# Performance work log

Measured on AMD Instinct MI355X. Metric: run time of the kernel, lower is better.

The kernel has to match this reference:

```python
import jax, jax.numpy as jnp
import numpy as np


def haar_dwt2d(x):
    """Orthonormal 2D Haar DWT. x: [B,C,H,W] -> (LL, LH, HL, HH) each [B,C,H/2,W/2].
    Matches conv2d(stride=2) with dec_lo=[1/sqrt2,1/sqrt2], dec_hi=[-1/sqrt2,1/sqrt2]."""
    x00 = x[:, :, 0::2, 0::2]
    x01 = x[:, :, 0::2, 1::2]
    x10 = x[:, :, 1::2, 0::2]
    x11 = x[:, :, 1::2, 1::2]
    LL = (x00 + x01 + x10 + x11) * 0.5
    LH = (x10 + x11 - x00 - x01) * 0.5  # high-pass along H
    HL = (x01 + x11 - x00 - x10) * 0.5  # high-pass along W
    HH = (x00 - x01 - x10 + x11) * 0.5
    return LL, LH, HL, HH


def haar_idwt2d(LL, LH, HL, HH):
    """Exact inverse of haar_dwt2d. Each input [B,C,h,w] -> [B,C,2h,2w]."""
    x00 = (LL - LH - HL + HH) * 0.5
    x01 = (LL - LH + HL - HH) * 0.5
    x10 = (LL + LH - HL - HH) * 0.5
    x11 = (LL + LH + HL + HH) * 0.5
    B, C, h, w = LL.shape
    row0 = jnp.stack([x00, x01], axis=-1).reshape(B, C, h, 2 * w)
    row1 = jnp.stack([x10, x11], axis=-1).reshape(B, C, h, 2 * w)
    return jnp.stack([row0, row1], axis=-2).reshape(B, C, 2 * h, 2 * w)


def _gate(t, thr):
    # scalar 0/1 gate: subband kept iff max|t| > thr (no grad through the gate)
    return (jnp.max(jnp.abs(t)) > thr).astype(t.dtype)


def reference(x):
    # WaveletTree: tree_level=8, sr_ratio=2, method='root', use_thres=True, threshold=1
    thr = jnp.asarray(1.0, dtype=x.dtype)

    LL1, LH1, HL1, HH1 = haar_dwt2d(x)
    LL2, LH2, HL2, HH2 = haar_dwt2d(LL1)
    LL3, LH3, HL3, HH3 = haar_dwt2d(LL2)

    # level-3 gates
    g3_lh = _gate(LH3, thr)
    g3_hl = _gate(HL3, thr)
    g3_hh = _gate(HH3, thr)
    out = haar_idwt2d(LL3, LH3 * g3_lh, HL3 * g3_hl, HH3 * g3_hh)

    # level-2 gates ('root' method: child kept only if parent was kept)
    thr2 = thr * 0.5
    g2_lh = _gate(LH2, thr2) * g3_lh
    g2_hl = _gate(HL2, thr2) * g3_hl
    g2_hh = _gate(HH2, thr2) * g3_hh
    out = haar_idwt2d(out, LH2 * g2_lh, HL2 * g2_hl, HH2 * g2_hh)

    # level-1 gated elementwise adds
    thr1 = thr * 0.25
    g1_lh = _gate(LH1, thr1) * g2_lh
    g1_hl = _gate(HL1, thr1) * g2_hl
    g1_hh = _gate(HH1, thr1) * g2_hh
    out = out + LH1 * g1_lh + HL1 * g1_hl + HH1 * g1_hh
    return out  # [B, C, H/2, W/2]


def setup_inputs() -> dict:
    key = jax.random.key(0)
    x = jax.random.normal(key, (8, 192, 224, 224), dtype=jnp.float32)
    return {"x": x}
```

## Files before the change

### kernel.cpp

```cpp
#include <hip/hip_runtime.h>


#define IMG_W 224
#define OUT_W 112
#define BANDS_PER_IMG 28
#define BAND_FLOATS 1792
#define OUT_BAND_FLOATS 448
#define NBG 1536
#define NBR 1024
#define WS_SLOTS 64

__device__ __forceinline__ void fwd_quad(float a, float b, float c, float d,
                                         float& ll, float& lh, float& hl, float& hh) {
    ll = (a + b + c + d) * 0.5f;
    lh = (c + d - a - b) * 0.5f;
    hl = (b + d - a - c) * 0.5f;
    hh = (a - b - c + d) * 0.5f;
}

__global__ __launch_bounds__(256, 6) void wav_gate_kernel(const float* __restrict__ x,
                                                          int* __restrict__ ws,
                                                          int n_bands) {
    const int lane = (int)threadIdx.x & 63;
    const int y = lane >> 4;
    const int j = lane & 15;
    const bool active = (j < 14);
    const int jc = active ? j : 0;
    const int wid = (int)blockIdx.x * 4 + ((int)threadIdx.x >> 6);
    const int nw = NBG * 4;

    float m[9];
#pragma unroll
    for (int k = 0; k < 9; ++k) m[k] = 0.0f;

    for (int bb = wid; bb < n_bands; bb += nw) {
        int b = n_bands - 1 - bb;
        const float* base = x + (size_t)b * BAND_FLOATS;
        const float* rowA = base + (2 * y) * IMG_W + jc * 4;
        const float* rowB = rowA + IMG_W;

        float4 A[4], B[4];
#pragma unroll
        for (int k = 0; k < 4; ++k) {
            A[k] = *reinterpret_cast<const float4*>(rowA + 56 * k);
            B[k] = *reinterpret_cast<const float4*>(rowB + 56 * k);
        }
        __builtin_amdgcn_sched_barrier(0);

        const bool bot = y & 1;
        const bool rp = (y >> 1) & 1;
        const bool cp = j & 1;
#pragma unroll
        for (int k = 0; k < 4; ++k) {
            float llp, lhv, hlv, hhv;
            fwd_quad(A[k].x, A[k].y, B[k].x, B[k].y, llp, lhv, hlv, hhv);
            m[0] = fmaxf(m[0], fabsf(lhv));
            m[1] = fmaxf(m[1], fabsf(hlv));
            m[2] = fmaxf(m[2], fabsf(hhv));
            float llq;
            fwd_quad(A[k].z, A[k].w, B[k].z, B[k].w, llq, lhv, hlv, hhv);
            m[0] = fmaxf(m[0], fabsf(lhv));
            m[1] = fmaxf(m[1], fabsf(hlv));
            m[2] = fmaxf(m[2], fabsf(hhv));
            float op = __shfl_xor(llp, 16);
            float oq = __shfl_xor(llq, 16);
            float a2 = bot ? op : llp, b2 = bot ? oq : llq;
            float c2 = bot ? llp : op, d2 = bot ? llq : oq;
            float ll2v;
            fwd_quad(a2, b2, c2, d2, ll2v, lhv, hlv, hhv);
            m[3] = fmaxf(m[3], fabsf(lhv));
            m[4] = fmaxf(m[4], fabsf(hlv));
            m[5] = fmaxf(m[5], fabsf(hhv));
            float nr = __shfl_xor(ll2v, 32);
            float nc = __shfl_xor(ll2v, 1);
            float nrc = __shfl_xor(ll2v, 33);
            float t   = rp ? nr  : ll2v;
            float tb  = rp ? ll2v : nr;
            float tn  = rp ? nrc : nc;
            float tbn = rp ? nc  : nrc;
            float a3 = cp ? tn : t,  b3 = cp ? t : tn;
            float c3 = cp ? tbn : tb, d3 = cp ? tb : tbn;
            float ll3;
            fwd_quad(a3, b3, c3, d3, ll3, lhv, hlv, hhv);
            m[6] = fmaxf(m[6], fabsf(lhv));
            m[7] = fmaxf(m[7], fabsf(hlv));
            m[8] = fmaxf(m[8], fabsf(hhv));
        }
    }

#pragma unroll
    for (int k = 0; k < 9; ++k) m[k] = active ? m[k] : 0.0f;

#pragma unroll
    for (int off = 32; off > 0; off >>= 1)
#pragma unroll
        for (int k = 0; k < 9; ++k) m[k] = fmaxf(m[k], __shfl_xor(m[k], off));

    __shared__ float red[4][9];
    int wv = (int)threadIdx.x >> 6;
    if (((int)threadIdx.x & 63) == 0) {
#pragma unroll
        for (int k = 0; k < 9; ++k) red[wv][k] = m[k];
    }
    __syncthreads();
    if (threadIdx.x == 0) {
        int slot = (int)blockIdx.x & (WS_SLOTS - 1);
#pragma unroll
        for (int k = 0; k < 9; ++k) {
            float vm = fmaxf(fmaxf(red[0][k], red[1][k]), fmaxf(red[2][k], red[3][k]));
            int vb = __float_as_int(vm);
            if (vb > ((volatile int*)ws)[slot * 9 + k]) atomicMax(&ws[slot * 9 + k], vb);
        }
    }
}

__global__ __launch_bounds__(256, 4) void wav_recon_kernel(const float* __restrict__ x,
                                                           const int* __restrict__ ws,
                                                           float* __restrict__ out,
                                                           int n_bands) {
    const int lane = (int)threadIdx.x & 63;
    float mx[9];
#pragma unroll
    for (int k = 0; k < 9; ++k) mx[k] = __int_as_float(ws[lane * 9 + k]);
#pragma unroll
    for (int off = 32; off > 0; off >>= 1)
#pragma unroll
        for (int k = 0; k < 9; ++k) mx[k] = fmaxf(mx[k], __shfl_xor(mx[k], off));

    const float g3lh = (mx[6] > 1.0f) ? 1.0f : 0.0f;
    const float g3hl = (mx[7] > 1.0f) ? 1.0f : 0.0f;
    const float g3hh = (mx[8] > 1.0f) ? 1.0f : 0.0f;
    const float g2lh = (mx[3] > 0.5f) ? g3lh : 0.0f;
    const float g2hl = (mx[4] > 0.5f) ? g3hl : 0.0f;
    const float g2hh = (mx[5] > 0.5f) ? g3hh : 0.0f;
    const float g1lh = (mx[0] > 0.25f) ? g2lh : 0.0f;
    const float g1hl = (mx[1] > 0.25f) ? g2hl : 0.0f;
    const float g1hh = (mx[2] > 0.25f) ? g2hh : 0.0f;

    const int y = lane >> 4;
    const int j = lane & 15;
    const bool active = (j < 14);
    const int jc = active ? j : 0;
    const int wid = (int)blockIdx.x * 4 + ((int)threadIdx.x >> 6);
    const int nw = NBR * 4;

    const bool bot = y & 1;
    const bool rp = (y >> 1) & 1;
    const bool cp = j & 1;
    const float sR = rp ? 1.0f : -1.0f;
    const float sC = cp ? 1.0f : -1.0f;
    const float sR1 = bot ? 1.0f : -1.0f;

    for (int b = wid; b < n_bands; b += nw) {
        const float* base = x + (size_t)b * BAND_FLOATS;
        const float* rowA = base + (2 * y) * IMG_W + jc * 4;
        const float* rowB = rowA + IMG_W;
        float* obase = out + (size_t)b * OUT_BAND_FLOATS + y * OUT_W;

        float4 A[4], B[4];
#pragma unroll
        for (int k = 0; k < 4; ++k) {
            A[k] = *reinterpret_cast<const float4*>(rowA + 56 * k);
            B[k] = *reinterpret_cast<const float4*>(rowB + 56 * k);
        }
        __builtin_amdgcn_sched_barrier(0);

#pragma unroll
        for (int k = 0; k < 4; ++k) {
            float llp, lh1p, hl1p, hh1p;
            fwd_quad(A[k].x, A[k].y, B[k].x, B[k].y, llp, lh1p, hl1p, hh1p);
            float llq, lh1q, hl1q, hh1q;
            fwd_quad(A[k].z, A[k].w, B[k].z, B[k].w, llq, lh1q, hl1q, hh1q);
            float op = __shfl_xor(llp, 16);
            float oq = __shfl_xor(llq, 16);
            float a2 = bot ? op : llp, b2 = bot ? oq : llq;
            float c2 = bot ? llp : op, d2 = bot ? llq : oq;
            float ll2v, lh2v, hl2v, hh2v;
            fwd_quad(a2, b2, c2, d2, ll2v, lh2v, hl2v, hh2v);
            float nr = __shfl_xor(ll2v, 32);
            float nc = __shfl_xor(ll2v, 1);
            float nrc = __shfl_xor(ll2v, 33);
            float t   = rp ? nr  : ll2v;
            float tb  = rp ? ll2v : nr;
            float tn  = rp ? nrc : nc;
            float tbn = rp ? nc  : nrc;
            float a3 = cp ? tn : t,  b3 = cp ? t : tn;
            float c3 = cp ? tbn : tb, d3 = cp ? tb : tbn;
            float ll3, lh3, hl3, hh3;
            fwd_quad(a3, b3, c3, d3, ll3, lh3, hl3, hh3);
            lh3 *= g3lh; hl3 *= g3hl; hh3 *= g3hh;
            float r2v = (ll3 + sR * lh3 + sC * hl3 + (sR * sC) * hh3) * 0.5f;
            float LH = lh2v * g2lh, HL = hl2v * g2hl, HH = hh2v * g2hh;
            float r1c0 = (r2v + sR1 * LH - HL - sR1 * HH) * 0.5f;
            float r1c1 = (r2v + sR1 * LH + HL + sR1 * HH) * 0.5f;
            float o0 = r1c0 + lh1p * g1lh + hl1p * g1hl + hh1p * g1hh;
            float o1 = r1c1 + lh1q * g1lh + hl1q * g1hl + hh1q * g1hh;
            if (active) {
                *reinterpret_cast<float2*>(obase + (14 * k + j) * 2) = make_float2(o0, o1);
            }
        }
    }
}

extern "C" void kernel_launch(void* const* d_in, const int* in_sizes, int n_in,
                              void* d_out, int out_size, void* d_ws, size_t ws_size,
                              hipStream_t stream) {
    const float* x = (const float*)d_in[0];
    float* out = (float*)d_out;
    int* ws = (int*)d_ws;

    int total = in_sizes[0];
    int n_img = total / (IMG_W * IMG_W);
    int n_bands = n_img * BANDS_PER_IMG;

    wav_gate_kernel<<<NBG, 256, 0, stream>>>(x, ws, n_bands);
    wav_recon_kernel<<<NBR, 256, 0, stream>>>(x, ws, out, n_bands);
}
```

Measured before the change: 491.0 us.

## Double-buffer band loads via async global-to-LDS staging in both kernels

Both kernels now stage each 8-row band into per-wave LDS buffers using global_load_lds and prefetch the next band while computing the current one, reading operands back with ds_read_b128. Block shape changes to 128 threads with 1280 blocks for both kernels. The aim is to hide global memory latency behind compute in this bandwidth-bound two-pass kernel, at the cost of LDS traffic, hand-written waitcnt assembly that depends on exact outstanding-load counts, and one redundant reload of the last band per wave.

```diff
diff --git a/kernel.cpp b/kernel.cpp
--- a/kernel.cpp
+++ b/kernel.cpp
@@ -1,14 +1,28 @@
 #include <hip/hip_runtime.h>
+#include <stdint.h>
 
 
 #define IMG_W 224
 #define OUT_W 112
-#define BANDS_PER_IMG 28
 #define BAND_FLOATS 1792
+#define BAND_BYTES 7168
 #define OUT_BAND_FLOATS 448
-#define NBG 1536
-#define NBR 1024
+#define NBLK 1280
+#define WPB 2
+#define NW (NBLK * WPB)
 #define WS_SLOTS 64
+
+#define DS_READ16(dst, addr, OFF) \
+    asm volatile("ds_read_b128 %0, %1 offset:" #OFF : "=&v"(dst) : "v"(addr))
+
+__device__ __forceinline__ void stage_band(const float* __restrict__ g, char* l, int lane) {
+#pragma unroll
+    for (int r = 0; r < 7; ++r) {
+        __builtin_amdgcn_global_load_lds(
+            (const __attribute__((address_space(1))) void*)(g + r * 256 + lane * 4),
+            (__attribute__((address_space(3))) void*)(l + r * 1024), 16, 0, 0);
+    }
+}
 
 __device__ __forceinline__ void fwd_quad(float a, float b, float c, float d,
                                          float& ll, float& lh, float& hl, float& hh) {
@@ -18,87 +32,96 @@
     hh = (a - b - c + d) * 0.5f;
 }
 
-__global__ __launch_bounds__(256, 6) void wav_gate_kernel(const float* __restrict__ x,
-                                                          int* __restrict__ ws,
-                                                          int n_bands) {
+__global__ __launch_bounds__(128) void wav_gate_kernel(const float* __restrict__ x,
+                                                       int* __restrict__ ws,
+                                                       int n_bands) {
+    __shared__ __align__(16) char lds[WPB * 2 * BAND_BYTES];
     const int lane = (int)threadIdx.x & 63;
+    const int wv = (int)threadIdx.x >> 6;
+    char* mybuf = lds + wv * (2 * BAND_BYTES);
+    const uint32_t lbase = (uint32_t)(uintptr_t)mybuf;
     const int y = lane >> 4;
     const int j = lane & 15;
     const bool active = (j < 14);
     const int jc = active ? j : 0;
-    const int wid = (int)blockIdx.x * 4 + ((int)threadIdx.x >> 6);
-    const int nw = NBG * 4;
+    const uint32_t lane_off = 1792u * (uint32_t)y + 16u * (uint32_t)jc;
+    const int wid = (int)blockIdx.x * WPB + wv;
 
     float m[9];
 #pragma unroll
     for (int k = 0; k < 9; ++k) m[k] = 0.0f;
 
-    for (int bb = wid; bb < n_bands; bb += nw) {
-        int b = n_bands - 1 - bb;
-        const float* base = x + (size_t)b * BAND_FLOATS;
-        const float* rowA = base + (2 * y) * IMG_W + jc * 4;
-        const float* rowB = rowA + IMG_W;
-
-        float4 A[4], B[4];
-#pragma unroll
-        for (int k = 0; k < 4; ++k) {
-            A[k] = *reinterpret_cast<const float4*>(rowA + 56 * k);
-            B[k] = *reinterpret_cast<const float4*>(rowB + 56 * k);
+    const bool bot = y & 1;
+    const bool rp = (y >> 1) & 1;
+    const bool cp = j & 1;
+
+    if (wid < n_bands) {
+        stage_band(x + (size_t)(n_bands - 1 - wid) * BAND_FLOATS, mybuf, lane);
+        int cur = 0;
+        for (int idx = wid; idx < n_bands; idx += NW) {
+            int nxt = idx + NW;
+            if (nxt >= n_bands) nxt = idx;
+            stage_band(x + (size_t)(n_bands - 1 - nxt) * BAND_FLOATS,
+                       mybuf + (cur ^ 1) * BAND_BYTES, lane);
+            asm volatile("s_waitcnt vmcnt(7)" ::: "memory");
+            uint32_t a = lbase + (uint32_t)(cur * BAND_BYTES) + lane_off;
+            float4 A[4], B[4];
+            DS_READ16(A[0], a, 0);    DS_READ16(A[1], a, 224);
+            DS_READ16(A[2], a, 448);  DS_READ16(A[3], a, 672);
+            DS_READ16(B[0], a, 896);  DS_READ16(B[1], a, 1120);
+            DS_READ16(B[2], a, 1344); DS_READ16(B[3], a, 1568);
+            asm volatile("s_waitcnt lgkmcnt(0)" ::: "memory");
+            __builtin_amdgcn_sched_barrier(0);
+
+#pragma unroll
+            for (int k = 0; k < 4; ++k) {
+                float llp, lhv, hlv, hhv;
+                fwd_quad(A[k].x, A[k].y, B[k].x, B[k].y, llp, lhv, hlv, hhv);
+                m[0] = fmaxf(m[0], fabsf(lhv));
+                m[1] = fmaxf(m[1], fabsf(hlv));
+                m[2] = fmaxf(m[2], fabsf(hhv));
+                float llq;
+                fwd_quad(A[k].z, A[k].w, B[k].z, B[k].w, llq, lhv, hlv, hhv);
+                m[0] = fmaxf(m[0], fabsf(lhv));
+                m[1] = fmaxf(m[1], fabsf(hlv));
+                m[2] = fmaxf(m[2], fabsf(hhv));
+                float op = __shfl_xor(llp, 16);
+                float oq = __shfl_xor(llq, 16);
+                float a2 = bot ? op : llp, b2 = bot ? oq : llq;
+                float c2 = bot ? llp : op, d2 = bot ? llq : oq;
+                float ll2v;
+                fwd_quad(a2, b2, c2, d2, ll2v, lhv, hlv, hhv);
+                m[3] = fmaxf(m[3], fabsf(lhv));
+                m[4] = fmaxf(m[4], fabsf(hlv));
+                m[5] = fmaxf(m[5], fabsf(hhv));
+                float nr = __shfl_xor(ll2v, 32);
+                float nc = __shfl_xor(ll2v, 1);
+                float nrc = __shfl_xor(ll2v, 33);
+                float t   = rp ? nr  : ll2v;
+                float tb  = rp ? ll2v : nr;
+                float tn  = rp ? nrc : nc;
+                float tbn = rp ? nc  : nrc;
+                float a3 = cp ? tn : t,  b3 = cp ? t : tn;
+                float c3 = cp ? tbn : tb, d3 = cp ? tb : tbn;
+                float ll3;
+                fwd_quad(a3, b3, c3, d3, ll3, lhv, hlv, hhv);
+                m[6] = fmaxf(m[6], fabsf(lhv));
+                m[7] = fmaxf(m[7], fabsf(hlv));
+                m[8] = fmaxf(m[8], fabsf(hhv));
+            }
+            cur ^= 1;
         }
-        __builtin_amdgcn_sched_barrier(0);
-
-        const bool bot = y & 1;
-        const bool rp = (y >> 1) & 1;
-        const bool cp = j & 1;
-#pragma unroll
-        for (int k = 0; k < 4; ++k) {
-            float llp, lhv, hlv, hhv;
-            fwd_quad(A[k].x, A[k].y, B[k].x, B[k].y, llp, lhv, hlv, hhv);
-            m[0] = fmaxf(m[0], fabsf(lhv));
-            m[1] = fmaxf(m[1], fabsf(hlv));
-            m[2] = fmaxf(m[2], fabsf(hhv));
-            float llq;
-            fwd_quad(A[k].z, A[k].w, B[k].z, B[k].w, llq, lhv, hlv, hhv);
-            m[0] = fmaxf(m[0], fabsf(lhv));
-            m[1] = fmaxf(m[1], fabsf(hlv));
-            m[2] = fmaxf(m[2], fabsf(hhv));
-            float op = __shfl_xor(llp, 16);
-            float oq = __shfl_xor(llq, 16);
-            float a2 = bot ? op : llp, b2 = bot ? oq : llq;
-            float c2 = bot ? llp : op, d2 = bot ? llq : oq;
-            float ll2v;
-            fwd_quad(a2, b2, c2, d2, ll2v, lhv, hlv, hhv);
-            m[3] = fmaxf(m[3], fabsf(lhv));
-            m[4] = fmaxf(m[4], fabsf(hlv));
-            m[5] = fmaxf(m[5], fabsf(hhv));
-            float nr = __shfl_xor(ll2v, 32);
-            float nc = __shfl_xor(ll2v, 1);
-            float nrc = __shfl_xor(ll2v, 33);
-            float t   = rp ? nr  : ll2v;
-            float tb  = rp ? ll2v : nr;
-            float tn  = rp ? nrc : nc;
-            float tbn = rp ? nc  : nrc;
-            float a3 = cp ? tn : t,  b3 = cp ? t : tn;
-            float c3 = cp ? tbn : tb, d3 = cp ? tb : tbn;
-            float ll3;
-            fwd_quad(a3, b3, c3, d3, ll3, lhv, hlv, hhv);
-            m[6] = fmaxf(m[6], fabsf(lhv));
-            m[7] = fmaxf(m[7], fabsf(hlv));
-            m[8] = fmaxf(m[8], fabsf(hhv));
-        }
     }
 
 #pragma unroll
     for (int k = 0; k < 9; ++k) m[k] = active ? m[k] : 0.0f;
-
 #pragma unroll
     for (int off = 32; off > 0; off >>= 1)
 #pragma unroll
         for (int k = 0; k < 9; ++k) m[k] = fmaxf(m[k], __shfl_xor(m[k], off));
 
-    __shared__ float red[4][9];
-    int wv = (int)threadIdx.x >> 6;
-    if (((int)threadIdx.x & 63) == 0) {
+    __shared__ float red[WPB][9];
+    if (lane == 0) {
 #pragma unroll
         for (int k = 0; k < 9; ++k) red[wv][k] = m[k];
     }
@@ -107,18 +130,23 @@
         int slot = (int)blockIdx.x & (WS_SLOTS - 1);
 #pragma unroll
         for (int k = 0; k < 9; ++k) {
-            float vm = fmaxf(fmaxf(red[0][k], red[1][k]), fmaxf(red[2][k], red[3][k]));
+            float vm = fmaxf(red[0][k], red[1][k]);
             int vb = __float_as_int(vm);
             if (vb > ((volatile int*)ws)[slot * 9 + k]) atomicMax(&ws[slot * 9 + k], vb);
         }
     }
 }
 
-__global__ __launch_bounds__(256, 4) void wav_recon_kernel(const float* __restrict__ x,
-                                                           const int* __restrict__ ws,
-                                                           float* __restrict__ out,
-                                                           int n_bands) {
+__global__ __launch_bounds__(128) void wav_recon_kernel(const float* __restrict__ x,
+                                                        const int* __restrict__ ws,
+                                                        float* __restrict__ out,
+                                                        int n_bands) {
+    __shared__ __align__(16) char lds[WPB * 2 * BAND_BYTES];
     const int lane = (int)threadIdx.x & 63;
+    const int wv = (int)threadIdx.x >> 6;
+    char* mybuf = lds + wv * (2 * BAND_BYTES);
+    const uint32_t lbase = (uint32_t)(uintptr_t)mybuf;
+
     float mx[9];
 #pragma unroll
     for (int k = 0; k < 9; ++k) mx[k] = __int_as_float(ws[lane * 9 + k]);
@@ -141,8 +169,8 @@
     const int j = lane & 15;
     const bool active = (j < 14);
     const int jc = active ? j : 0;
-    const int wid = (int)blockIdx.x * 4 + ((int)threadIdx.x >> 6);
-    const int nw = NBR * 4;
+    const uint32_t lane_off = 1792u * (uint32_t)y + 16u * (uint32_t)jc;
+    const int wid = (int)blockIdx.x * WPB + wv;
 
     const bool bot = y & 1;
     const bool rp = (y >> 1) & 1;
@@ -151,53 +179,59 @@
     const float sC = cp ? 1.0f : -1.0f;
     const float sR1 = bot ? 1.0f : -1.0f;
 
-    for (int b = wid; b < n_bands; b += nw) {
-        const float* base = x + (size_t)b * BAND_FLOATS;
-        const float* rowA = base + (2 * y) * IMG_W + jc * 4;
-        const float* rowB = rowA + IMG_W;
-        float* obase = out + (size_t)b * OUT_BAND_FLOATS + y * OUT_W;
-
-        float4 A[4], B[4];
-#pragma unroll
-        for (int k = 0; k < 4; ++k) {
-            A[k] = *reinterpret_cast<const float4*>(rowA + 56 * k);
-            B[k] = *reinterpret_cast<const float4*>(rowB + 56 * k);
-        }
-        __builtin_amdgcn_sched_barrier(0);
-
-#pragma unroll
-        for (int k = 0; k < 4; ++k) {
-            float llp, lh1p, hl1p, hh1p;
-            fwd_quad(A[k].x, A[k].y, B[k].x, B[k].y, llp, lh1p, hl1p, hh1p);
-            float llq, lh1q, hl1q, hh1q;
-            fwd_quad(A[k].z, A[k].w, B[k].z, B[k].w, llq, lh1q, hl1q, hh1q);
-            float op = __shfl_xor(llp, 16);
-            float oq = __shfl_xor(llq, 16);
-            float a2 = bot ? op : llp, b2 = bot ? oq : llq;
-            float c2 = bot ? llp : op, d2 = bot ? llq : oq;
-            float ll2v, lh2v, hl2v, hh2v;
-            fwd_quad(a2, b2, c2, d2, ll2v, lh2v, hl2v, hh2v);
-            float nr = __shfl_xor(ll2v, 32);
-            float nc = __shfl_xor(ll2v, 1);
-            float nrc = __shfl_xor(ll2v, 33);
-            float t   = rp ? nr  : ll2v;
-            float tb  = rp ? ll2v : nr;
-            float tn  = rp ? nrc : nc;
-            float tbn = rp ? nc  : nrc;
-            float a3 = cp ? tn : t,  b3 = cp ? t : tn;
-            float c3 = cp ? tbn : tb, d3 = cp ? tb : tbn;
-            float ll3, lh3, hl3, hh3;
-            fwd_quad(a3, b3, c3, d3, ll3, lh3, hl3, hh3);
-            lh3 *= g3lh; hl3 *= g3hl; hh3 *= g3hh;
-            float r2v = (ll3 + sR * lh3 + sC * hl3 + (sR * sC) * hh3) * 0.5f;
-            float LH = lh2v * g2lh, HL = hl2v * g2hl, HH = hh2v * g2hh;
-            float r1c0 = (r2v + sR1 * LH - HL - sR1 * HH) * 0.5f;
-            float r1c1 = (r2v + sR1 * LH + HL + sR1 * HH) * 0.5f;
-            float o0 = r1c0 + lh1p * g1lh + hl1p * g1hl + hh1p * g1hh;
-            float o1 = r1c1 + lh1q * g1lh + hl1q * g1hl + hh1q * g1hh;
-            if (active) {
-                *reinterpret_cast<float2*>(obase + (14 * k + j) * 2) = make_float2(o0, o1);
+    if (wid < n_bands) {
+        stage_band(x + (size_t)wid * BAND_FLOATS, mybuf, lane);
+        int cur = 0;
+        for (int idx = wid; idx < n_bands; idx += NW) {
+            int nxt = idx + NW;
+            if (nxt >= n_bands) nxt = idx;
+            stage_band(x + (size_t)nxt * BAND_FLOATS, mybuf + (cur ^ 1) * BAND_BYTES, lane);
+            asm volatile("s_waitcnt vmcnt(7)" ::: "memory");
+            uint32_t a = lbase + (uint32_t)(cur * BAND_BYTES) + lane_off;
+            float4 A[4], B[4];
+            DS_READ16(A[0], a, 0);    DS_READ16(A[1], a, 224);
+            DS_READ16(A[2], a, 448);  DS_READ16(A[3], a, 672);
+            DS_READ16(B[0], a, 896);  DS_READ16(B[1], a, 1120);
+            DS_READ16(B[2], a, 1344); DS_READ16(B[3], a, 1568);
+            asm volatile("s_waitcnt lgkmcnt(0)" ::: "memory");
+            __builtin_amdgcn_sched_barrier(0);
+
+            float* obase = out + (size_t)idx * OUT_BAND_FLOATS + y * OUT_W;
+#pragma unroll
+            for (int k = 0; k < 4; ++k) {
+                float llp, lh1p, hl1p, hh1p;
+                fwd_quad(A[k].x, A[k].y, B[k].x, B[k].y, llp, lh1p, hl1p, hh1p);
+                float llq, lh1q, hl1q, hh1q;
+                fwd_quad(A[k].z, A[k].w, B[k].z, B[k].w, llq, lh1q, hl1q, hh1q);
+                float op = __shfl_xor(llp, 16);
+                float oq = __shfl_xor(llq, 16);
+                float a2 = bot ? op : llp, b2 = bot ? oq : llq;
+                float c2 = bot ? llp : op, d2 = bot ? llq : oq;
+                float ll2v, lh2v, hl2v, hh2v;
+                fwd_quad(a2, b2, c2, d2, ll2v, lh2v, hl2v, hh2v);
+                float nr = __shfl_xor(ll2v, 32);
+                float nc = __shfl_xor(ll2v, 1);
+                float nrc = __shfl_xor(ll2v, 33);
+                float t   = rp ? nr  : ll2v;
+                float tb  = rp ? ll2v : nr;
+                float tn  = rp ? nrc : nc;
+                float tbn = rp ? nc  : nrc;
+                float a3 = cp ? tn : t,  b3 = cp ? t : tn;
+                float c3 = cp ? tbn : tb, d3 = cp ? tb : tbn;
+                float ll3, lh3, hl3, hh3;
+                fwd_quad(a3, b3, c3, d3, ll3, lh3, hl3, hh3);
+                lh3 *= g3lh; hl3 *= g3hl; hh3 *= g3hh;
+                float r2v = (ll3 + sR * lh3 + sC * hl3 + (sR * sC) * hh3) * 0.5f;
+                float LH = lh2v * g2lh, HL = hl2v * g2hl, HH = hh2v * g2hh;
+                float r1c0 = (r2v + sR1 * LH - HL - sR1 * HH) * 0.5f;
+                float r1c1 = (r2v + sR1 * LH + HL + sR1 * HH) * 0.5f;
+                float o0 = r1c0 + lh1p * g1lh + hl1p * g1hl + hh1p * g1hh;
+                float o1 = r1c1 + lh1q * g1lh + hl1q * g1hl + hh1q * g1hh;
+                if (active) {
+                    *reinterpret_cast<float2*>(obase + (14 * k + j) * 2) = make_float2(o0, o1);
+                }
             }
+            cur ^= 1;
         }
     }
 }
@@ -211,8 +245,8 @@
 
     int total = in_sizes[0];
     int n_img = total / (IMG_W * IMG_W);
-    int n_bands = n_img * BANDS_PER_IMG;
-
-    wav_gate_kernel<<<NBG, 256, 0, stream>>>(x, ws, n_bands);
-    wav_recon_kernel<<<NBR, 256, 0, stream>>>(x, ws, out, n_bands);
-}
+    int n_bands = n_img * (IMG_W / 8);
+
+    wav_gate_kernel<<<NBLK, 128, 0, stream>>>(x, ws, n_bands);
+    wav_recon_kernel<<<NBLK, 128, 0, stream>>>(x, ws, out, n_bands);
+}
```

Measured after the change: 488.8 us. About the same (-0.4%).
